# Kernel optimization log

Measured on AMD Instinct MI355X. Metric: run time of the kernel, lower is better.

Reference implementation:

```python
import jax, jax.numpy as jnp
import numpy as np


def setup_inputs() -> dict:
    key = jax.random.key(0)
    k1, k2, k3 = jax.random.split(key, 3)
    B, L, D, K = 8, 4096, 1024, 4
    x = jax.random.normal(k1, (B, L, D), dtype=jnp.float32)
    w = jax.random.normal(k2, (D, 1, K), dtype=jnp.float32) * (1.0 / np.sqrt(K))
    b = jax.random.normal(k3, (D,), dtype=jnp.float32) * 0.02
    return {"x": x, "w": w, "b": b}


def reference(x, w, b):
    # x: (B, L, D); w: (D, 1, K) depthwise kernel; b: (D,)
    D = x.shape[-1]
    K = w.shape[-1]
    pad = K - 1
    xc = jnp.transpose(x, (0, 2, 1))  # (B, D, L)
    # torch pads both sides by pad then slices off trailing pad -> left-only causal pad
    y = jax.lax.conv_general_dilated(
        xc, w,
        window_strides=(1,),
        padding=[(pad, 0)],
        dimension_numbers=("NCH", "OIH", "NCH"),
        feature_group_count=D,
    )
    y = y + b[None, :, None]
    return jnp.transpose(y, (0, 2, 1))  # (B, L, D)
```

## Files before the change

### kernel.cpp

```cpp
#include <hip/hip_runtime.h>

typedef float float4v __attribute__((ext_vector_type(4)));

#define TL 16
#define K  4

__global__ __launch_bounds__(256) void cconv_kernel(
    const float* __restrict__ x,
    const float* __restrict__ w,
    const float* __restrict__ bias,
    float* __restrict__ y,
    int B, int L, int D)
{
    const int DG = D >> 2;
    const int NT = L / TL;
    int tid  = blockIdx.x * blockDim.x + threadIdx.x;
    int dg   = tid % DG;
    int rest = tid / DG;
    int lt   = rest % NT;
    int b    = rest / NT;
    if (b >= B) return;

    const int d0 = dg << 2;

    float wv[K][4];
    {
        const float4v* wp = reinterpret_cast<const float4v*>(w + (size_t)d0 * K);
        #pragma unroll
        for (int j = 0; j < 4; ++j) {
            float4v v = wp[j];
            #pragma unroll
            for (int k = 0; k < K; ++k) wv[k][j] = v[k];
        }
    }
    float4v bv = *reinterpret_cast<const float4v*>(bias + d0);

    const int    l0   = lt * TL;
    const size_t base = (size_t)b * L * D + d0;

    float4v xm3 = {0.f, 0.f, 0.f, 0.f};
    float4v xm2 = {0.f, 0.f, 0.f, 0.f};
    float4v xm1 = {0.f, 0.f, 0.f, 0.f};

    if (l0 >= 3) {
        xm3 = *reinterpret_cast<const float4v*>(x + base + (size_t)(l0 - 3) * D);
        xm2 = *reinterpret_cast<const float4v*>(x + base + (size_t)(l0 - 2) * D);
        xm1 = *reinterpret_cast<const float4v*>(x + base + (size_t)(l0 - 1) * D);
    }

    #pragma unroll
    for (int t = 0; t < TL; ++t) {
        const int l = l0 + t;
        float4v xc = *reinterpret_cast<const float4v*>(x + base + (size_t)l * D);

        float4v out;
        #pragma unroll
        for (int j = 0; j < 4; ++j) {
            float acc = bv[j];
            acc = fmaf(wv[0][j], xm3[j], acc);
            acc = fmaf(wv[1][j], xm2[j], acc);
            acc = fmaf(wv[2][j], xm1[j], acc);
            acc = fmaf(wv[3][j], xc[j],  acc);
            out[j] = acc;
        }
        __builtin_nontemporal_store(out,
            reinterpret_cast<float4v*>(y + base + (size_t)l * D));

        xm3 = xm2; xm2 = xm1; xm1 = xc;
    }
}

extern "C" void kernel_launch(void* const* d_in, const int* in_sizes, int n_in,
                              void* d_out, int out_size, void* d_ws, size_t ws_size,
                              hipStream_t stream) {
    const float* x  = (const float*)d_in[0];
    const float* w  = (const float*)d_in[1];
    const float* bb = (const float*)d_in[2];
    float* y        = (float*)d_out;

    const int D = in_sizes[2];
    const int L = 4096;
    const int B = in_sizes[0] / (L * D);

    const int threads = B * (L / TL) * (D / 4);
    const int block   = 256;
    const int grid    = (threads + block - 1) / block;

    cconv_kernel<<<grid, block, 0, stream>>>(x, w, bb, y, B, L, D);
}
```

Baseline: 48.27 us.

## Remap blocks per XCD, narrow to float2 channels and lengthen time tiles

Blocks are remapped so that consecutive logical blocks land on the same XCD, which should improve L2 locality for the overlapping halo rows. Each thread now handles two channels with float2 loads and stores instead of four with float4, and the time tile grows from 16 to 64 steps with partial unrolling. The longer tile cuts the redundant halo reads, while the narrower vectors give more threads per row. The risk is lower bytes per memory instruction and fewer total threads (64 tiles per sequence instead of 256). The XCD remap assumes the grid divides evenly by 8.

```diff
diff --git a/kernel.cpp b/kernel.cpp
--- a/kernel.cpp
+++ b/kernel.cpp
@@ -1,61 +1,64 @@
 #include <hip/hip_runtime.h>
 
+typedef float float2v __attribute__((ext_vector_type(2)));
 typedef float float4v __attribute__((ext_vector_type(4)));
 
-#define TL 16
-#define K  4
+#define TL   64
+#define K    4
+#define NXCD 8
 
 __global__ __launch_bounds__(256) void cconv_kernel(
     const float* __restrict__ x,
     const float* __restrict__ w,
     const float* __restrict__ bias,
     float* __restrict__ y,
-    int B, int L, int D)
+    int B, int L, int D, int cpx)
 {
-    const int DG = D >> 2;
+    const int blk = (int)(blockIdx.x % NXCD) * cpx + (int)(blockIdx.x / NXCD);
+
+    const int DG = D >> 1;
     const int NT = L / TL;
-    int tid  = blockIdx.x * blockDim.x + threadIdx.x;
+    int tid  = blk * (int)blockDim.x + (int)threadIdx.x;
     int dg   = tid % DG;
     int rest = tid / DG;
     int lt   = rest % NT;
     int b    = rest / NT;
     if (b >= B) return;
 
-    const int d0 = dg << 2;
+    const int d0 = dg << 1;
 
-    float wv[K][4];
+    float wv[K][2];
     {
-        const float4v* wp = reinterpret_cast<const float4v*>(w + (size_t)d0 * K);
         #pragma unroll
-        for (int j = 0; j < 4; ++j) {
-            float4v v = wp[j];
+        for (int j = 0; j < 2; ++j) {
+            float4v v = *reinterpret_cast<const float4v*>(w + (size_t)(d0 + j) * K);
             #pragma unroll
             for (int k = 0; k < K; ++k) wv[k][j] = v[k];
         }
     }
-    float4v bv = *reinterpret_cast<const float4v*>(bias + d0);
+    float2v bv = *reinterpret_cast<const float2v*>(bias + d0);
 
     const int    l0   = lt * TL;
     const size_t base = (size_t)b * L * D + d0;
 
-    float4v xm3 = {0.f, 0.f, 0.f, 0.f};
-    float4v xm2 = {0.f, 0.f, 0.f, 0.f};
-    float4v xm1 = {0.f, 0.f, 0.f, 0.f};
+    float2v xm3 = {0.f, 0.f};
+    float2v xm2 = {0.f, 0.f};
+    float2v xm1 = {0.f, 0.f};
 
     if (l0 >= 3) {
-        xm3 = *reinterpret_cast<const float4v*>(x + base + (size_t)(l0 - 3) * D);
-        xm2 = *reinterpret_cast<const float4v*>(x + base + (size_t)(l0 - 2) * D);
-        xm1 = *reinterpret_cast<const float4v*>(x + base + (size_t)(l0 - 1) * D);
+        xm3 = *reinterpret_cast<const float2v*>(x + base + (size_t)(l0 - 3) * D);
+        xm2 = *reinterpret_cast<const float2v*>(x + base + (size_t)(l0 - 2) * D);
+        xm1 = *reinterpret_cast<const float2v*>(x + base + (size_t)(l0 - 1) * D);
     }
 
-    #pragma unroll
+    #pragma unroll 8
     for (int t = 0; t < TL; ++t) {
         const int l = l0 + t;
-        float4v xc = *reinterpret_cast<const float4v*>(x + base + (size_t)l * D);
+        float2v xc = *reinterpret_cast<const float2v*>(x + base + (size_t)l * D);
 
-        float4v out;
+        float2v out;
         #pragma unroll
-        for (int j = 0; j < 4; ++j) {
+        for (int j = 0; j < 2; ++j) {
             float acc = bv[j];
             acc = fmaf(wv[0][j], xm3[j], acc);
             acc = fmaf(wv[1][j], xm2[j], acc);
@@ -64,7 +67,7 @@
             out[j] = acc;
         }
         __builtin_nontemporal_store(out,
-            reinterpret_cast<float4v*>(y + base + (size_t)l * D));
+            reinterpret_cast<float2v*>(y + base + (size_t)l * D));
 
         xm3 = xm2; xm2 = xm1; xm1 = xc;
     }
@@ -82,9 +85,10 @@
     const int L = 4096;
     const int B = in_sizes[0] / (L * D);
 
-    const int threads = B * (L / TL) * (D / 4);
+    const int threads = B * (L / TL) * (D / 2);
     const int block   = 256;
     const int grid    = (threads + block - 1) / block;
+    const int cpx     = grid / NXCD;
 
-    cconv_kernel<<<grid, block, 0, stream>>>(x, w, bb, y, B, L, D);
+    cconv_kernel<<<grid, block, 0, stream>>>(x, w, bb, y, B, L, D, cpx);
 }
```

New measurement: 44.27 us. -8.3%, faster.
